# Kernel optimization log

Hardware: AMD Instinct MI355X
Metric: run time of the kernel (lower is better)

Reference implementation:

```python
import jax, jax.numpy as jnp
import numpy as np

L, D, H, FF, V, A, CTX, B, S = 6, 768, 12, 3072, 51865, 1500, 448, 32, 8
DH = D // H


def _ln(x, w, b, eps=1e-5):
    m = x.mean(-1, keepdims=True)
    v = ((x - m) ** 2).mean(-1, keepdims=True)
    return (x - m) * jax.lax.rsqrt(v + eps) * w + b


def _mha(q, k, v, mask=None):
    # q: [B,Sq,D], k/v: [B,T,D]
    b, sq, _ = q.shape
    t = k.shape[1]
    q = q.reshape(b, sq, H, DH)
    k = k.reshape(b, t, H, DH)
    v = v.reshape(b, t, H, DH)
    w = jnp.einsum('bsnd,btnd->bnst', q, k) * (DH ** -0.5)
    if mask is not None:
        w = w + mask
    w = jax.nn.softmax(w, axis=-1)
    return jnp.einsum('bnst,btnd->bsnd', w, v).reshape(b, sq, D)


def _forward(tokens, audio_features, token_emb, pos_emb, attn_ln_w, attn_ln_b,
             Wq, bq, Wk, Wv, bv, Wo, bo, cross_ln_w, cross_ln_b,
             cWq, cbq, cWk, cWv, cbv, cWo, cbo, mlp_ln_w, mlp_ln_b,
             W1, b1, W2, b2, ln_w, ln_b):
    s = tokens.shape[1]
    x = token_emb[tokens] + pos_emb[:s]  # [B,S,D]
    i_ = jnp.arange(s)
    mask = jnp.where(i_[None, :] > i_[:, None], -jnp.inf, 0.0).astype(x.dtype)
    for i in range(L):
        h = _ln(x, attn_ln_w[i], attn_ln_b[i])
        x = x + _mha(h @ Wq[i] + bq[i], h @ Wk[i], h @ Wv[i] + bv[i], mask) @ Wo[i] + bo[i]
        h = _ln(x, cross_ln_w[i], cross_ln_b[i])
        x = x + _mha(h @ cWq[i] + cbq[i], audio_features @ cWk[i],
                     audio_features @ cWv[i] + cbv[i]) @ cWo[i] + cbo[i]
        h = _ln(x, mlp_ln_w[i], mlp_ln_b[i])
        x = x + jax.nn.gelu(h @ W1[i] + b1[i], approximate=False) @ W2[i] + b2[i]
    x = _ln(x, ln_w, ln_b)
    return x @ token_emb.T  # [B,S,V]


def setup_inputs() -> dict:
    key = jax.random.key(0)
    ks = iter(jax.random.split(key, 40))
    def rn(shape, scale=0.02):
        return jax.random.normal(next(ks), shape, jnp.float32) * scale
    return {
        'tokens': jax.random.randint(next(ks), (B, S), 0, V),
        'audio_features': jax.random.normal(next(ks), (B, A, D), jnp.float32),
        'token_emb': rn((V, D)),
        'pos_emb': rn((CTX, D)),
        'attn_ln_w': jnp.ones((L, D)), 'attn_ln_b': jnp.zeros((L, D)),
        'Wq': rn((L, D, D)), 'bq': jnp.zeros((L, D)),
        'Wk': rn((L, D, D)),
        'Wv': rn((L, D, D)), 'bv': jnp.zeros((L, D)),
        'Wo': rn((L, D, D)), 'bo': jnp.zeros((L, D)),
        'cross_ln_w': jnp.ones((L, D)), 'cross_ln_b': jnp.zeros((L, D)),
        'cWq': rn((L, D, D)), 'cbq': jnp.zeros((L, D)),
        'cWk': rn((L, D, D)),
        'cWv': rn((L, D, D)), 'cbv': jnp.zeros((L, D)),
        'cWo': rn((L, D, D)), 'cbo': jnp.zeros((L, D)),
        'mlp_ln_w': jnp.ones((L, D)), 'mlp_ln_b': jnp.zeros((L, D)),
        'W1': rn((L, D, FF)), 'b1': jnp.zeros((L, FF)),
        'W2': rn((L, FF, D)), 'b2': jnp.zeros((L, D)),
        'ln_w': jnp.ones((D,)), 'ln_b': jnp.zeros((D,)),
    }


def reference(tokens, audio_features, token_emb, pos_emb, attn_ln_w, attn_ln_b,
              Wq, bq, Wk, Wv, bv, Wo, bo, cross_ln_w, cross_ln_b,
              cWq, cbq, cWk, cWv, cbv, cWo, cbo, mlp_ln_w, mlp_ln_b,
              W1, b1, W2, b2, ln_w, ln_b):
    return _forward(tokens, audio_features, token_emb, pos_emb, attn_ln_w, attn_ln_b,
                    Wq, bq, Wk, Wv, bv, Wo, bo, cross_ln_w, cross_ln_b,
                    cWq, cbq, cWk, cWv, cbv, cWo, cbo, mlp_ln_w, mlp_ln_b,
                    W1, b1, W2, b2, ln_w, ln_b)
```

## Files before the change

### kernel.cpp

```cpp
#include <hip/hip_runtime.h>
#include <hip/hip_bf16.h>

#define HH 12
#define DD 768
#define FFD 3072
#define AAn 1500
#define BBn 32
#define RR 256
#define VV 51865
#define VPAD2 52224
#define MAT (768*768)
#define LSTR ((size_t)8 * MAT + 2 * (size_t)DD * FFD)
#define TPAD 1536

#define OP_BIAS 1
#define OP_GELU 2
#define OP_RES  4
#define OP_BF16 8
#define OP_SCAT 16

typedef float f32x4 __attribute__((ext_vector_type(4)));
typedef short s16x8 __attribute__((ext_vector_type(8)));

__device__ __forceinline__ unsigned short f2bf(float f) {
  union { float f; unsigned int u; } v; v.f = f;
  unsigned int r = (v.u + 0x7fffu + ((v.u >> 16) & 1u)) >> 16;
  return (unsigned short)r;
}
__device__ __forceinline__ float bf2f_lo(unsigned int u) {
  union { unsigned int u; float f; } v; v.u = u << 16; return v.f;
}
__device__ __forceinline__ float bf2f_hi(unsigned int u) {
  union { unsigned int u; float f; } v; v.u = u & 0xffff0000u; return v.f;
}

__device__ __forceinline__ void gld_lds16(const unsigned short* g, unsigned short* l) {
  __builtin_amdgcn_global_load_lds(
      (const __attribute__((address_space(1))) void*)g,
      (__attribute__((address_space(3))) void*)l, 16, 0, 0);
}

__global__ __launch_bounds__(256) void embed_ln_k(
    const int* __restrict__ toks, const float* __restrict__ emb,
    const float* __restrict__ pos, const float* __restrict__ w,
    const float* __restrict__ b, float* __restrict__ x,
    unsigned short* __restrict__ out) {
  int r = blockIdx.x;
  int s8 = r & 7;
  int tk = toks[r];
  int t = threadIdx.x;
  float v[3];
  #pragma unroll
  for (int j = 0; j < 3; j++) {
    int c = t + j * 256;
    float nv = emb[(size_t)tk * DD + c] + pos[(size_t)s8 * DD + c];
    x[(size_t)r * DD + c] = nv;
    v[j] = nv;
  }
  float s = v[0] + v[1] + v[2];
  for (int o = 32; o; o >>= 1) s += __shfl_down(s, o);
  __shared__ float red[4], red2[4];
  int wid = t >> 6, lane = t & 63;
  if (!lane) red[wid] = s;
  __syncthreads();
  float mean = (red[0] + red[1] + red[2] + red[3]) * (1.f / DD);
  float d0 = v[0] - mean, d1 = v[1] - mean, d2 = v[2] - mean;
  float s2 = d0 * d0 + d1 * d1 + d2 * d2;
  for (int o = 32; o; o >>= 1) s2 += __shfl_down(s2, o);
  if (!lane) red2[wid] = s2;
  __syncthreads();
  float var = (red2[0] + red2[1] + red2[2] + red2[3]) * (1.f / DD);
  float rstd = rsqrtf(var + 1e-5f);
  out[(size_t)r * DD + t]       = f2bf(d0 * rstd * w[t] + b[t]);
  out[(size_t)r * DD + t + 256] = f2bf(d1 * rstd * w[t + 256] + b[t + 256]);
  out[(size_t)r * DD + t + 512] = f2bf(d2 * rstd * w[t + 512] + b[t + 512]);
}

__global__ void cvt_bf16v(const float* __restrict__ src, unsigned short* __restrict__ dst,
                          long long n_src, long long n_tot) {
  long long g = ((long long)blockIdx.x * 256 + threadIdx.x) * 8;
  long long stride = (long long)gridDim.x * 256 * 8;
  for (; g < n_tot; g += stride) {
    union { unsigned short us[8]; s16x8 v; } pk;
    if (g + 8 <= n_src) {
      float4 f0 = *(const float4*)(src + g);
      float4 f1 = *(const float4*)(src + g + 4);
      pk.us[0] = f2bf(f0.x); pk.us[1] = f2bf(f0.y); pk.us[2] = f2bf(f0.z); pk.us[3] = f2bf(f0.w);
      pk.us[4] = f2bf(f1.x); pk.us[5] = f2bf(f1.y); pk.us[6] = f2bf(f1.z); pk.us[7] = f2bf(f1.w);
    } else {
      #pragma unroll
      for (int i = 0; i < 8; i++)
        pk.us[i] = (g + i < n_src) ? f2bf(src[g + i]) : (unsigned short)0;
    }
    *(s16x8*)(dst + g) = pk.v;
  }
}

__global__ void build_biases(const float* __restrict__ bq, const float* __restrict__ bv,
                             float* __restrict__ qkvb) {
  int i = blockIdx.x * 256 + threadIdx.x;
  if (i < 6 * 2304) {
    int l = i / 2304, n = i % 2304;
    qkvb[i] = (n < 768) ? bq[l * 768 + n] : (n < 1536 ? 0.f : bv[l * 768 + (n - 1536)]);
  }
}

__global__ __launch_bounds__(256) void red_resid_ln(
    const float* __restrict__ part, int nparts, const float* __restrict__ bias,
    float* __restrict__ x, const float* __restrict__ w,
    const float* __restrict__ b, unsigned short* __restrict__ out) {
  int row = blockIdx.x;
  int t = threadIdx.x;
  float v[3];
  #pragma unroll
  for (int j = 0; j < 3; j++) {
    int c = t + j * 256;
    size_t i = (size_t)row * DD + c;
    float nv = x[i] + bias[c];
    for (int p = 0; p < nparts; p++) nv += part[(size_t)p * RR * DD + i];
    x[i] = nv;
    v[j] = nv;
  }
  float s = v[0] + v[1] + v[2];
  for (int o = 32; o; o >>= 1) s += __shfl_down(s, o);
  __shared__ float red[4], red2[4];
  int wid = t >> 6, lane = t & 63;
  if (!lane) red[wid] = s;
  __syncthreads();
  float mean = (red[0] + red[1] + red[2] + red[3]) * (1.f / DD);
  float d0 = v[0] - mean, d1 = v[1] - mean, d2 = v[2] - mean;
  float s2 = d0 * d0 + d1 * d1 + d2 * d2;
  for (int o = 32; o; o >>= 1) s2 += __shfl_down(s2, o);
  if (!lane) red2[wid] = s2;
  __syncthreads();
  float var = (red2[0] + red2[1] + red2[2] + red2[3]) * (1.f / DD);
  float rstd = rsqrtf(var + 1e-5f);
  out[(size_t)row * DD + t]       = f2bf(d0 * rstd * w[t] + b[t]);
  out[(size_t)row * DD + t + 256] = f2bf(d1 * rstd * w[t + 256] + b[t + 256]);
  out[(size_t)row * DD + t + 512] = f2bf(d2 * rstd * w[t + 512] + b[t + 512]);
}

struct WPtrs { const float* p[10]; };
__global__ __launch_bounds__(256) void transpose_w(
    WPtrs wp, unsigned short* __restrict__ dst) {
  int l = blockIdx.y;
  int idx = blockIdx.x;
  int zz, ct, rt, R, C;
  if (idx < 1152)      { zz = idx / 144; int t = idx % 144; ct = t % 12; rt = t / 12; R = DD; C = DD; }
  else if (idx < 1728) { zz = 8; int t = idx - 1152; ct = t % 48; rt = t / 48; R = DD; C = FFD; }
  else                 { zz = 9; int t = idx - 1728; rt = t % 48; ct = t / 48; R = FFD; C = DD; }
  const float* W = wp.p[zz] + (size_t)l * ((zz < 8) ? MAT : (size_t)DD * FFD);
  size_t doff = (zz < 8) ? (size_t)zz * MAT
                         : ((zz == 8) ? (size_t)8 * MAT : (size_t)8 * MAT + (size_t)FFD * DD);
  unsigned short* Wt = dst + (size_t)l * LSTR + doff;
  __shared__ unsigned short tile[64][65];
  int r0 = rt * 64, c0 = ct * 64;
  int tid = threadIdx.x;
  int rr = tid >> 3, cc = (tid & 7) * 8;
  #pragma unroll
  for (int j = 0; j < 2; j++) {
    int r = r0 + j * 32 + rr;
    const float* sp = W + (size_t)r * C + c0 + cc;
    float4 f0 = *(const float4*)sp, f1 = *(const float4*)(sp + 4);
    unsigned short* tp = &tile[j * 32 + rr][cc];
    tp[0] = f2bf(f0.x); tp[1] = f2bf(f0.y); tp[2] = f2bf(f0.z); tp[3] = f2bf(f0.w);
    tp[4] = f2bf(f1.x); tp[5] = f2bf(f1.y); tp[6] = f2bf(f1.z); tp[7] = f2bf(f1.w);
  }
  __syncthreads();
  #pragma unroll
  for (int j = 0; j < 2; j++) {
    int c = c0 + j * 32 + rr;
    union { unsigned short us[8]; s16x8 v; } pk;
    #pragma unroll
    for (int i = 0; i < 8; i++) pk.us[i] = tile[cc + i][j * 32 + rr];
    *(s16x8*)&Wt[(size_t)c * R + r0 + cc] = pk.v;
  }
}

__global__ __launch_bounds__(256) void audio_prep(
    const float* __restrict__ audio, unsigned short* __restrict__ a_bf,
    unsigned short* __restrict__ aT) {
  int b = blockIdx.z;
  int t0 = blockIdx.x * 64, e0 = blockIdx.y * 64;
  __shared__ unsigned short tile[64][65];
  int tid = threadIdx.x;
  const float* src = audio + (size_t)b * AAn * DD;
  unsigned short* dstb = a_bf + (size_t)b * AAn * DD;
  int rr = tid >> 3, cc = (tid & 7) * 8;
  #pragma unroll
  for (int j = 0; j < 2; j++) {
    int t = t0 + j * 32 + rr;
    union { unsigned short us[8]; s16x8 v; } pk;
    if (t < AAn) {
      const float* sp = src + (size_t)t * DD + e0 + cc;
      float4 f0 = *(const float4*)sp, f1 = *(const float4*)(sp + 4);
      pk.us[0] = f2bf(f0.x); pk.us[1] = f2bf(f0.y); pk.us[2] = f2bf(f0.z); pk.us[3] = f2bf(f0.w);
      pk.us[4] = f2bf(f1.x); pk.us[5] = f2bf(f1.y); pk.us[6] = f2bf(f1.z); pk.us[7] = f2bf(f1.w);
      *(s16x8*)&dstb[(size_t)t * DD + e0 + cc] = pk.v;
    } else {
      #pragma unroll
      for (int i = 0; i < 8; i++) pk.us[i] = 0;
    }
    unsigned short* tp = &tile[j * 32 + rr][cc];
    #pragma unroll
    for (int i = 0; i < 8; i++) tp[i] = pk.us[i];
  }
  __syncthreads();
  unsigned short* dstT = aT + (size_t)b * DD * TPAD;
  #pragma unroll
  for (int j = 0; j < 2; j++) {
    int e = e0 + j * 32 + rr;
    union { unsigned short us[8]; s16x8 v; } pk;
    #pragma unroll
    for (int i = 0; i < 8; i++) pk.us[i] = tile[cc + i][j * 32 + rr];
    *(s16x8*)&dstT[(size_t)e * TPAD + t0 + cc] = pk.v;
  }
}

template <int BM, int BN>
__global__ __launch_bounds__(256, 2) void gemm_t(
    const unsigned short* __restrict__ A, const unsigned short* __restrict__ Bt,
    void* __restrict__ Cv, const float* __restrict__ bias,
    const float* __restrict__ resid, int Klen, int Kstride, int Nout, int Cld,
    long zsA, long zsB, long zsC, long zsBias, int kz, int gmap, int op) {
  constexpr int WM = BM / 2, WN = BN / 2;
  constexpr int MREP = WM / 16, NREP = WN / 16;
  __shared__ unsigned short As[BM * 64];
  __shared__ unsigned short Bs[BN * 64];
  int bx = blockIdx.x, by = blockIdx.y, bz = blockIdx.z;
  if (gmap == 1) { int t = bx; bx = bz; bz = t; }
  else if (gmap == 2) {
    int id = bx;
    bx = (id >> 4) * 8 + (id & 7);
    by = (id >> 3) & 1;
    bz = 0;
  } else if (gmap == 3) {
    int id = bx;
    bx = ((id >> 5) << 3) | (id & 7);
    by = (id >> 3) & 3;
    bz = 0;
  }
  const int n0 = bx * BN, m0 = by * BM;
  const int z = bz;
  const int kbeg = kz ? z * Klen : 0;
  const int tid = threadIdx.x, w = tid >> 6, l = tid & 63;
  const int wr = w >> 1, wc = w & 1;
  f32x4 acc[MREP][NREP] = {};

  const int rowA = l >> 3;
  const int colK = (l & 7) * 8;
  const unsigned short* gA =
      A + (size_t)z * zsA + (size_t)(m0 + w * (BM / 4) + rowA) * Kstride + colK + kbeg;
  const unsigned short* gB =
      Bt + (size_t)z * zsB + (size_t)(n0 + w * (BN / 4) + rowA) * Kstride + colK + kbeg;

  for (int k0 = 0; k0 < Klen; k0 += 64) {
    __syncthreads();
    #pragma unroll
    for (int p = 0; p < BM / 32; p++)
      gld_lds16(gA + (size_t)(p * 8) * Kstride + k0, &As[(w * (BM / 4) + p * 8) * 64]);
    #pragma unroll
    for (int p = 0; p < BN / 32; p++)
      gld_lds16(gB + (size_t)(p * 8) * Kstride + k0, &Bs[(w * (BN / 4) + p * 8) * 64]);
    __syncthreads();
    #pragma unroll
    for (int kk = 0; kk < 2; kk++) {
      s16x8 aF[MREP], bF[NREP];
      #pragma unroll
      for (int m = 0; m < MREP; m++)
        aF[m] = *(const s16x8*)&As[(wr * WM + m * 16 + (l & 15)) * 64 + kk * 32 + (l >> 4) * 8];
      #pragma unroll
      for (int n = 0; n < NREP; n++)
        bF[n] = *(const s16x8*)&Bs[(wc * WN + n * 16 + (l & 15)) * 64 + kk * 32 + (l >> 4) * 8];
      #pragma unroll
      for (int m = 0; m < MREP; m++)
        #pragma unroll
        for (int n = 0; n < NREP; n++)
          acc[m][n] = __builtin_amdgcn_mfma_f32_16x16x32_bf16(aF[m], bF[n], acc[m][n], 0, 0, 0);
    }
  }

  const float* biasz = (op & OP_BIAS) ? bias + (size_t)z * zsBias : nullptr;
  #pragma unroll
  for (int m = 0; m < MREP; m++) {
    int rr0 = m0 + wr * WM + m * 16 + (l >> 4) * 4;
    #pragma unroll
    for (int n = 0; n < NREP; n++) {
      int c = n0 + wc * WN + n * 16 + (l & 15);
      if (c < Nout) {
        float bval = (op & OP_BIAS) ? biasz[c] : 0.f;
        #pragma unroll
        for (int j = 0; j < 4; j++) {
          int r = rr0 + j;
          float val = acc[m][n][j] + bval;
          if (op & OP_GELU) val = 0.5f * val * (1.f + erff(val * 0.70710678118f));
          if (op & OP_RES)  val += resid[(size_t)r * Cld + c];
          if (op & OP_SCAT) {
            int hh = r >> 3;
            if (hh < HH)
              ((unsigned short*)Cv)[((size_t)hh * 256 + z * 8 + (r & 7)) * 768 + c] = f2bf(val);
          } else if (op & OP_BF16) {
            ((unsigned short*)Cv)[(size_t)z * zsC + (size_t)r * Cld + c] = f2bf(val);
          } else {
            ((float*)Cv)[(size_t)z * zsC + (size_t)r * Cld + c] = val;
          }
        }
      }
    }
  }
}

__global__ __launch_bounds__(64) void self_attn_k(
    const float* __restrict__ qkv, unsigned short* __restrict__ out) {
  int bh = blockIdx.x;
  int b = bh / HH, h = bh % HH;
  __shared__ float qs[8][65], ks[8][65], vs[8][65], ps[8][9];
  int l = threadIdx.x;
  for (int s = 0; s < 8; s++) {
    size_t base = ((size_t)(b * 8 + s)) * 2304 + h * 64 + l;
    qs[s][l] = qkv[base]; ks[s][l] = qkv[base + 768]; vs[s][l] = qkv[base + 1536];
  }
  __syncthreads();
  int s = l >> 3, t = l & 7;
  float sc = 0.f;
  #pragma unroll
  for (int d = 0; d < 64; d++) sc += qs[s][d] * ks[t][d];
  sc *= 0.125f;
  if (t > s) sc = -1e30f;
  float mx = sc;
  for (int o = 4; o; o >>= 1) mx = fmaxf(mx, __shfl_xor(mx, o, 8));
  float e = __expf(sc - mx);
  float sum = e;
  for (int o = 4; o; o >>= 1) sum += __shfl_xor(sum, o, 8);
  ps[s][t] = e / sum;
  __syncthreads();
  for (int s2 = 0; s2 < 8; s2++) {
    float acc = 0.f;
    #pragma unroll
    for (int t2 = 0; t2 < 8; t2++) acc += ps[s2][t2] * vs[t2][l];
    out[((size_t)(b * 8 + s2)) * DD + h * 64 + l] = f2bf(acc);
  }
}

__global__ __launch_bounds__(256) void qprime_k(
    const float* __restrict__ p2, const float* __restrict__ cbq,
    const float* __restrict__ cWk, unsigned short* __restrict__ Qp) {
  int bh = blockIdx.x;
  int b = bh / HH, h = bh % HH;
  __shared__ float qs[8][64];
  int tid = threadIdx.x;
  for (int i = tid; i < 512; i += 256) {
    int s = i >> 6, d = i & 63;
    size_t idx = (size_t)(b * 8 + s) * 768 + h * 64 + d;
    float acc = cbq[h * 64 + d];
    #pragma unroll
    for (int p = 0; p < 6; p++) acc += p2[(size_t)p * RR * DD + idx];
    qs[s][d] = acc * 0.125f;
  }
  __syncthreads();
  for (int e = tid; e < 768; e += 256) {
    const float* wr = cWk + (size_t)e * 768 + h * 64;
    float acc[8] = {};
    #pragma unroll 16
    for (int k = 0; k < 64; k++) {
      float wv = wr[k];
      #pragma unroll
      for (int s = 0; s < 8; s++) acc[s] += qs[s][k] * wv;
    }
    #pragma unroll
    for (int s = 0; s < 8; s++)
      Qp[((size_t)b * 128 + h * 8 + s) * 768 + e] = f2bf(acc[s]);
  }
}

__global__ __launch_bounds__(256) void xsoftmax_k(
    const unsigned short* __restrict__ S, unsigned short* __restrict__ P) {
  int bh = blockIdx.x;
  int b = bh / HH, h = bh % HH;
  int w = threadIdx.x >> 6, ln = threadIdx.x & 63;
  for (int rr = w; rr < 8; rr += 4) {
    size_t row = (size_t)b * 128 + h * 8 + rr;
    const unsigned int* sr = (const unsigned int*)(S + row * TPAD);
    unsigned int* pr = (unsigned int*)(P + row * TPAD);
    float v[24];
    float mx = -1e30f;
    #pragma unroll
    for (int i = 0; i < 12; i++) {
      unsigned int u = sr[ln + i * 64];
      int t0 = 2 * (ln + i * 64);
      v[2 * i]     = (t0 < AAn)     ? bf2f_lo(u) : -1e30f;
      v[2 * i + 1] = (t0 + 1 < AAn) ? bf2f_hi(u) : -1e30f;
      mx = fmaxf(mx, fmaxf(v[2 * i], v[2 * i + 1]));
    }
    for (int o = 32; o; o >>= 1) mx = fmaxf(mx, __shfl_xor(mx, o));
    float sum = 0.f;
    #pragma unroll
    for (int i = 0; i < 24; i++) { v[i] = __expf(v[i] - mx); sum += v[i]; }
    for (int o = 32; o; o >>= 1) sum += __shfl_xor(sum, o);
    float inv = 1.f / sum;
    #pragma unroll
    for (int i = 0; i < 12; i++) {
      int t0 = 2 * (ln + i * 64);
      unsigned int lo = (t0 < AAn)     ? f2bf(v[2 * i] * inv)     : 0;
      unsigned int hi = (t0 + 1 < AAn) ? f2bf(v[2 * i + 1] * inv) : 0;
      pr[ln + i * 64] = lo | (hi << 16);
    }
  }
}

static inline void* carve(char*& p, size_t bytes) {
  void* r = p;
  p += (bytes + 255) & ~(size_t)255;
  return r;
}

extern "C" void kernel_launch(void* const* d_in, const int* in_sizes, int n_in,
                              void* d_out, int out_size, void* d_ws, size_t ws_size,
                              hipStream_t stream) {
  const int*   tokens = (const int*)d_in[0];
  const float* audio  = (const float*)d_in[1];
  const float* temb   = (const float*)d_in[2];
  const float* pemb   = (const float*)d_in[3];
  const float* aln_w  = (const float*)d_in[4];
  const float* aln_b  = (const float*)d_in[5];
  const float* Wq = (const float*)d_in[6];
  const float* bq = (const float*)d_in[7];
  const float* Wk = (const float*)d_in[8];
  const float* Wv = (const float*)d_in[9];
  const float* bv = (const float*)d_in[10];
  const float* Wo = (const float*)d_in[11];
  const float* bo = (const float*)d_in[12];
  const float* cln_w = (const float*)d_in[13];
  const float* cln_b = (const float*)d_in[14];
  const float* cWq = (const float*)d_in[15];
  const float* cbq = (const float*)d_in[16];
  const float* cWk = (const float*)d_in[17];
  const float* cWv = (const float*)d_in[18];
  const float* cbv = (const float*)d_in[19];
  const float* cWo = (const float*)d_in[20];
  const float* cbo = (const float*)d_in[21];
  const float* mln_w = (const float*)d_in[22];
  const float* mln_b = (const float*)d_in[23];
  const float* W1 = (const float*)d_in[24];
  const float* b1 = (const float*)d_in[25];
  const float* W2 = (const float*)d_in[26];
  const float* b2 = (const float*)d_in[27];
  const float* lnw = (const float*)d_in[28];
  const float* lnb = (const float*)d_in[29];

  char* cur = (char*)d_ws;
  float* x    = (float*)carve(cur, (size_t)RR * DD * 4);
  float* qkv  = (float*)carve(cur, (size_t)RR * 2304 * 4);
  unsigned short* hb    = (unsigned short*)carve(cur, (size_t)RR * DD * 2);
  unsigned short* attnb = (unsigned short*)carve(cur, (size_t)RR * DD * 2);
  unsigned short* ffb   = (unsigned short*)carve(cur, (size_t)RR * FFD * 2);
  unsigned short* wt    = (unsigned short*)carve(cur, LSTR * 6 * 2);
  unsigned short* audio_bf = (unsigned short*)carve(cur, (size_t)BBn * AAn * DD * 2);
  unsigned short* audioT   = (unsigned short*)carve(cur, (size_t)BBn * DD * TPAD * 2);
  unsigned short* emb_bf = (unsigned short*)carve(cur, (size_t)VPAD2 * DD * 2);
  unsigned short* Sb = (unsigned short*)carve(cur, (size_t)BBn * 128 * TPAD * 2);
  unsigned short* Pb  = (unsigned short*)carve(cur, (size_t)BBn * 128 * TPAD * 2);
  unsigned short* Qp  = (unsigned short*)carve(cur, (size_t)BBn * 128 * DD * 2);
  unsigned short* Rbf = (unsigned short*)carve(cur, (size_t)HH * 256 * DD * 2);
  float* qkvb  = (float*)carve(cur, (size_t)6 * 2304 * 4);
  float* mlp2p = (float*)carve(cur, (size_t)8 * RR * DD * 4);

  auto G64 = [&](const unsigned short* A_, const unsigned short* Bt_, void* C_,
                 const float* bias_, const float* res_, int M_, int Np_,
                 int Klen_, int Kstr_, int Nout_, int Cld_, int op_,
                 int Z_ = 1, long zsA_ = 0, long zsB_ = 0, long zsC_ = 0,
                 long zsBias_ = 0, int kz_ = 0) {
    dim3 g(Np_ / 64, M_ / 64, Z_);
    gemm_t<64, 64><<<g, 256, 0, stream>>>(A_, Bt_, C_, bias_, res_,
        Klen_, Kstr_, Nout_, Cld_, zsA_, zsB_, zsC_, zsBias_, kz_, 0, op_);
  };
  auto G32 = [&](const unsigned short* A_, const unsigned short* Bt_, void* C_,
                 const float* bias_, const float* res_, int M_, int Np_,
                 int Klen_, int Kstr_, int Nout_, int Cld_, int op_,
                 int Z_ = 1, long zsA_ = 0, long zsB_ = 0, long zsC_ = 0,
                 long zsBias_ = 0, int kz_ = 0) {
    dim3 g(Np_ / 32, M_ / 32, Z_);
    gemm_t<32, 32><<<g, 256, 0, stream>>>(A_, Bt_, C_, bias_, res_,
        Klen_, Kstr_, Nout_, Cld_, zsA_, zsB_, zsC_, zsBias_, kz_, 0, op_);
  };

  embed_ln_k<<<RR, 256, 0, stream>>>(tokens, temb, pemb, aln_w, aln_b, x, hb);
  audio_prep<<<dim3(24, 12, BBn), 256, 0, stream>>>(audio, audio_bf, audioT);
  cvt_bf16v<<<4096, 256, 0, stream>>>(temb, emb_bf,
      (long long)VV * DD, (long long)VPAD2 * DD);
  build_biases<<<54, 256, 0, stream>>>(bq, bv, qkvb);

  WPtrs wp;
  wp.p[0] = Wq; wp.p[1] = Wk; wp.p[2] = Wv; wp.p[3] = Wo;
  wp.p[4] = cWq; wp.p[5] = cWk; wp.p[6] = cWv; wp.p[7] = cWo;
  wp.p[8] = W1; wp.p[9] = W2;
  transpose_w<<<dim3(2304, 6, 1), 256, 0, stream>>>(wp, wt);

  for (int l = 0; l < 6; l++) {
    size_t vD = (size_t)l * DD;
    size_t vF = (size_t)l * FFD;
    unsigned short* wtl = wt + (size_t)l * LSTR;

    G32(hb, wtl, qkv, qkvb + (size_t)l * 2304, nullptr, RR, 2304, DD, DD, 2304, 2304, OP_BIAS);
    self_attn_k<<<BBn * HH, 64, 0, stream>>>(qkv, attnb);
    G64(attnb, wtl + (size_t)3 * MAT, mlp2p, nullptr, nullptr, RR, DD, 128, DD, DD, DD,
        0, 6, 0, 0, (long)RR * DD, 0, 1);
    red_resid_ln<<<RR, 256, 0, stream>>>(mlp2p, 6, bo + vD, x, cln_w + vD, cln_b + vD, hb);

    G64(hb, wtl + (size_t)4 * MAT, mlp2p, nullptr, nullptr, RR, DD, 128, DD, DD, DD,
        0, 6, 0, 0, (long)RR * DD, 0, 1);
    qprime_k<<<BBn * HH, 256, 0, stream>>>(mlp2p, cbq + vD, cWk + (size_t)l * MAT, Qp);
    {
      dim3 g(BBn, 1, TPAD / 64);
      gemm_t<128, 64><<<g, 256, 0, stream>>>(Qp, audio_bf, Sb, nullptr,
          nullptr, DD, DD, TPAD, TPAD, (long)128 * DD, (long)AAn * DD,
          (long)128 * TPAD, 0, 0, 1, OP_BF16);
    }
    xsoftmax_k<<<BBn * HH, 256, 0, stream>>>(Sb, Pb);
    {
      dim3 g(BBn, 1, DD / 32);
      gemm_t<128, 32><<<g, 256, 0, stream>>>(Pb, audioT, Rbf, nullptr,
          nullptr, TPAD, TPAD, DD, DD, (long)128 * TPAD, (long)DD * TPAD, 0, 0, 0, 1, OP_SCAT);
    }
    G32(Rbf, wtl + (size_t)6 * MAT, attnb, cbv + vD, nullptr, RR, 64, DD, DD, 64, DD,
        OP_BIAS | OP_BF16, HH, (long)256 * DD, (long)64 * DD, 64, 64, 0);
    G64(attnb, wtl + (size_t)7 * MAT, mlp2p, nullptr, nullptr, RR, DD, 128, DD, DD, DD,
        0, 6, 0, 0, (long)RR * DD, 0, 1);
    red_resid_ln<<<RR, 256, 0, stream>>>(mlp2p, 6, cbo + vD, x, mln_w + vD, mln_b + vD, hb);

    G32(hb, wtl + (size_t)8 * MAT, ffb, b1 + vF, nullptr, RR, FFD, DD, DD, FFD, FFD,
        OP_BIAS | OP_GELU | OP_BF16);
    G64(ffb, wtl + (size_t)8 * MAT + (size_t)DD * FFD, mlp2p, nullptr, nullptr,
        RR, DD, 384, FFD, DD, DD, 0, 8, 0, 0, (long)RR * DD, 0, 1);
    const float* nw = (l < 5) ? (aln_w + (size_t)(l + 1) * DD) : lnw;
    const float* nb = (l < 5) ? (aln_b + (size_t)(l + 1) * DD) : lnb;
    red_resid_ln<<<RR, 256, 0, stream>>>(mlp2p, 8, b2 + vD, x, nw, nb, hb);
  }

  {
    dim3 g(1632, 1, 1);
    gemm_t<64, 128><<<g, 256, 0, stream>>>(hb, emb_bf, d_out, nullptr,
        nullptr, DD, DD, VV, VV, 0, 0, 0, 0, 0, 3, 0);
  }
}
```

Baseline: 1.280 ms.

## Use row-major audio directly in P·V GEMM, dropping transposed audio copy

Removes the audio_prep kernel that built a transposed bf16 copy of the audio features and replaces it with a plain bf16 conversion. A new pv_nt kernel computes P·audio using the row-major audio buffer, loading B tiles of 64 time steps by 32 features and gathering MFMA B fragments with strided LDS reads. This removes a large transpose write and its memory footprint, at the cost of strided, possibly bank-conflicting LDS reads for the B operand in each of the six per-layer PV GEMMs.

Measured after the change: 1.270 ms. About the same (-0.8%).

```diff
diff --git a/kernel.cpp b/kernel.cpp
--- a/kernel.cpp
+++ b/kernel.cpp
@@ -174,46 +174,6 @@
     #pragma unroll
     for (int i = 0; i < 8; i++) pk.us[i] = tile[cc + i][j * 32 + rr];
     *(s16x8*)&Wt[(size_t)c * R + r0 + cc] = pk.v;
-  }
-}
-
-__global__ __launch_bounds__(256) void audio_prep(
-    const float* __restrict__ audio, unsigned short* __restrict__ a_bf,
-    unsigned short* __restrict__ aT) {
-  int b = blockIdx.z;
-  int t0 = blockIdx.x * 64, e0 = blockIdx.y * 64;
-  __shared__ unsigned short tile[64][65];
-  int tid = threadIdx.x;
-  const float* src = audio + (size_t)b * AAn * DD;
-  unsigned short* dstb = a_bf + (size_t)b * AAn * DD;
-  int rr = tid >> 3, cc = (tid & 7) * 8;
-  #pragma unroll
-  for (int j = 0; j < 2; j++) {
-    int t = t0 + j * 32 + rr;
-    union { unsigned short us[8]; s16x8 v; } pk;
-    if (t < AAn) {
-      const float* sp = src + (size_t)t * DD + e0 + cc;
-      float4 f0 = *(const float4*)sp, f1 = *(const float4*)(sp + 4);
-      pk.us[0] = f2bf(f0.x); pk.us[1] = f2bf(f0.y); pk.us[2] = f2bf(f0.z); pk.us[3] = f2bf(f0.w);
-      pk.us[4] = f2bf(f1.x); pk.us[5] = f2bf(f1.y); pk.us[6] = f2bf(f1.z); pk.us[7] = f2bf(f1.w);
-      *(s16x8*)&dstb[(size_t)t * DD + e0 + cc] = pk.v;
-    } else {
-      #pragma unroll
-      for (int i = 0; i < 8; i++) pk.us[i] = 0;
-    }
-    unsigned short* tp = &tile[j * 32 + rr][cc];
-    #pragma unroll
-    for (int i = 0; i < 8; i++) tp[i] = pk.us[i];
-  }
-  __syncthreads();
-  unsigned short* dstT = aT + (size_t)b * DD * TPAD;
-  #pragma unroll
-  for (int j = 0; j < 2; j++) {
-    int e = e0 + j * 32 + rr;
-    union { unsigned short us[8]; s16x8 v; } pk;
-    #pragma unroll
-    for (int i = 0; i < 8; i++) pk.us[i] = tile[cc + i][j * 32 + rr];
-    *(s16x8*)&dstT[(size_t)e * TPAD + t0 + cc] = pk.v;
   }
 }
 
@@ -306,6 +266,66 @@
           }
         }
       }
+    }
+  }
+}
+
+__global__ __launch_bounds__(256, 2) void pv_nt(
+    const unsigned short* __restrict__ P, const unsigned short* __restrict__ audio_bf,
+    unsigned short* __restrict__ Rbf) {
+  __shared__ unsigned short As[128 * 64];
+  __shared__ unsigned short Bs[64 * 32];
+  const int b = blockIdx.x, et = blockIdx.z;
+  const int n0 = et * 32;
+  const int tid = threadIdx.x, w = tid >> 6, l = tid & 63;
+  const int wr = w >> 1, wc = w & 1;
+  f32x4 acc[4] = {};
+
+  const int rowA = l >> 3;
+  const int colK = (l & 7) * 8;
+  const unsigned short* gA =
+      P + (size_t)b * 128 * TPAD + (size_t)(w * 32 + rowA) * TPAD + colK;
+  const int tloc = w * 16 + (l >> 2);
+  const int eoff = (l & 3) * 8;
+  const unsigned short* gBbase = audio_bf + (size_t)b * AAn * DD;
+
+  for (int k0 = 0; k0 < TPAD; k0 += 64) {
+    __syncthreads();
+    #pragma unroll
+    for (int p = 0; p < 4; p++)
+      gld_lds16(gA + (size_t)(p * 8) * TPAD + k0, &As[(w * 32 + p * 8) * 64]);
+    {
+      int tg = k0 + tloc;
+      if (tg >= AAn) tg = AAn - 1;
+      gld_lds16(gBbase + (size_t)tg * DD + n0 + eoff, &Bs[w * 512]);
+    }
+    __syncthreads();
+    #pragma unroll
+    for (int kk = 0; kk < 2; kk++) {
+      s16x8 aF[4];
+      #pragma unroll
+      for (int m = 0; m < 4; m++)
+        aF[m] = *(const s16x8*)&As[(wr * 64 + m * 16 + (l & 15)) * 64 + kk * 32 + (l >> 4) * 8];
+      union { unsigned short us[8]; s16x8 v; } bF;
+      #pragma unroll
+      for (int i = 0; i < 8; i++)
+        bF.us[i] = Bs[(kk * 32 + (l >> 4) * 8 + i) * 32 + wc * 16 + (l & 15)];
+      #pragma unroll
+      for (int m = 0; m < 4; m++)
+        acc[m] = __builtin_amdgcn_mfma_f32_16x16x32_bf16(aF[m], bF.v, acc[m], 0, 0, 0);
+    }
+  }
+
+  #pragma unroll
+  for (int m = 0; m < 4; m++) {
+    int rr0 = wr * 64 + m * 16 + (l >> 4) * 4;
+    int c = n0 + wc * 16 + (l & 15);
+    #pragma unroll
+    for (int j = 0; j < 4; j++) {
+      int r = rr0 + j;
+      int hh = r >> 3;
+      if (hh < HH)
+        Rbf[((size_t)hh * 256 + b * 8 + (r & 7)) * 768 + c] = f2bf(acc[m][j]);
     }
   }
 }
@@ -456,7 +476,6 @@
   unsigned short* ffb   = (unsigned short*)carve(cur, (size_t)RR * FFD * 2);
   unsigned short* wt    = (unsigned short*)carve(cur, LSTR * 6 * 2);
   unsigned short* audio_bf = (unsigned short*)carve(cur, (size_t)BBn * AAn * DD * 2);
-  unsigned short* audioT   = (unsigned short*)carve(cur, (size_t)BBn * DD * TPAD * 2);
   unsigned short* emb_bf = (unsigned short*)carve(cur, (size_t)VPAD2 * DD * 2);
   unsigned short* Sb = (unsigned short*)carve(cur, (size_t)BBn * 128 * TPAD * 2);
   unsigned short* Pb  = (unsigned short*)carve(cur, (size_t)BBn * 128 * TPAD * 2);
@@ -485,7 +504,8 @@
   };
 
   embed_ln_k<<<RR, 256, 0, stream>>>(tokens, temb, pemb, aln_w, aln_b, x, hb);
-  audio_prep<<<dim3(24, 12, BBn), 256, 0, stream>>>(audio, audio_bf, audioT);
+  cvt_bf16v<<<4096, 256, 0, stream>>>(audio, audio_bf,
+      (long long)BBn * AAn * DD, (long long)BBn * AAn * DD);
   cvt_bf16v<<<4096, 256, 0, stream>>>(temb, emb_bf,
       (long long)VV * DD, (long long)VPAD2 * DD);
   build_biases<<<54, 256, 0, stream>>>(bq, bv, qkvb);
@@ -519,8 +539,7 @@
     xsoftmax_k<<<BBn * HH, 256, 0, stream>>>(Sb, Pb);
     {
       dim3 g(BBn, 1, DD / 32);
-      gemm_t<128, 32><<<g, 256, 0, stream>>>(Pb, audioT, Rbf, nullptr,
-          nullptr, TPAD, TPAD, DD, DD, (long)128 * TPAD, (long)DD * TPAD, 0, 0, 0, 1, OP_SCAT);
+      pv_nt<<<g, 256, 0, stream>>>(Pb, audio_bf, Rbf);
     }
     G32(Rbf, wtl + (size_t)6 * MAT, attnb, cbv + vD, nullptr, RR, 64, DD, DD, 64, DD,
         OP_BIAS | OP_BF16, HH, (long)256 * DD, (long)64 * DD, 64, 64, 0);
```
